# Optimization experiments

Measured on AMD Instinct MI355X. Metric: run time of the kernel, lower is better.

Reference implementation:

```python
import jax, jax.numpy as jnp
import numpy as np
from functools import reduce

N_QUBITS = 5
DIM = 2 ** N_QUBITS  # 32


def _cnot_np(c, t):
    # CNOT on N_QUBITS qubits, wire 0 = most significant bit (deepquantum convention)
    M = np.zeros((DIM, DIM), np.complex64)
    for i in range(DIM):
        if (i >> (N_QUBITS - 1 - c)) & 1:
            j = i ^ (1 << (N_QUBITS - 1 - t))
        else:
            j = i
        M[j, i] = 1.0
    return M

_CNOT = {(c, t): jnp.asarray(_cnot_np(c, t))
         for c in range(N_QUBITS) for t in range(N_QUBITS) if c != t}
_EYE2 = jnp.eye(2, dtype=jnp.complex64)


def _ry(theta):
    c = jnp.cos(theta / 2).astype(jnp.complex64)
    s = jnp.sin(theta / 2).astype(jnp.complex64)
    return jnp.stack([jnp.stack([c, -s]), jnp.stack([s, c])])


def _rx(theta):
    c = jnp.cos(theta / 2).astype(jnp.complex64)
    s = jnp.sin(theta / 2).astype(jnp.complex64)
    js = jnp.complex64(1j) * s
    return jnp.stack([jnp.stack([c, -js]), jnp.stack([-js, c])])


def _layer(gate_fn, thetas, wires):
    # kron of single-qubit gates on `wires`, identity elsewhere
    mats, idx = [], 0
    for w in range(N_QUBITS):
        if w in wires:
            mats.append(gate_fn(thetas[idx])); idx += 1
        else:
            mats.append(_EYE2)
    return reduce(jnp.kron, mats)


def _build_circuit(params, wires):
    # params: (n_blocks, 2, len(wires)); block = rylayer, rxlayer, then CNOTs
    # with control = block index and targets = all other wires in increasing order
    U = jnp.eye(DIM, dtype=jnp.complex64)
    n_blocks = params.shape[0]
    for b in range(n_blocks):
        U = _layer(_ry, params[b, 0], wires) @ U
        U = _layer(_rx, params[b, 1], wires) @ U
        for t in wires:
            if t != b:
                U = _CNOT[(b, t)] @ U
    return U


def setup_inputs() -> dict:
    key = jax.random.key(0)
    k1, k2, k3 = jax.random.split(key, 3)
    B = 65536
    oracles = jax.random.normal(k1, (B, DIM, DIM), dtype=jnp.float32)
    params1 = jax.random.normal(k2, (5, 2, 5), dtype=jnp.float32)  # cir1: 5 blocks, ry+rx, 5 wires
    params2 = jax.random.normal(k3, (4, 2, 4), dtype=jnp.float32)  # cir2: 4 blocks, ry+rx, wires [0,1,2,3]
    return {"oracles": oracles, "params1": params1, "params2": params2}


def reference(oracles, params1, params2):
    U1 = _build_circuit(params1, [0, 1, 2, 3, 4])
    U2 = _build_circuit(params2, [0, 1, 2, 3])
    psi1 = U1[:, 0]  # cir1 applied to |00000>
    mid = jnp.einsum('bij,j->bi', oracles.astype(jnp.complex64), psi1)  # oracle application (batched)
    fin = jnp.einsum('ij,bj->bi', U2, mid)                              # cir2
    x = jnp.abs(fin[:, 0]) ** 2 + jnp.abs(fin[:, 1]) ** 2
    return jnp.stack([x, 1.0 - x], axis=-1)  # (B, 2)
```

## Files before the change

### kernel.cpp

```cpp
#include <hip/hip_runtime.h>
#include <math.h>


__device__ __forceinline__ void apply_ry(float c, float s, int mask, int lane,
                                         float& re, float& im) {
    float pre = __shfl_xor(re, mask, 64);
    float pim = __shfl_xor(im, mask, 64);
    float sg = (lane & mask) ? s : -s;
    re = c * re + sg * pre;
    im = c * im + sg * pim;
}

__device__ __forceinline__ void apply_rx(float c, float s, int mask,
                                         float& re, float& im) {
    float pre = __shfl_xor(re, mask, 64);
    float pim = __shfl_xor(im, mask, 64);
    float nre = c * re + s * pim;
    float nim = c * im - s * pre;
    re = nre; im = nim;
}

__device__ __forceinline__ void apply_cnot(int cmask, int tmask, int lane,
                                           float& re, float& im) {
    float pre = __shfl_xor(re, tmask, 64);
    float pim = __shfl_xor(im, tmask, 64);
    if (lane & cmask) { re = pre; im = pim; }
}

__device__ __forceinline__ void u2row(const float* __restrict__ p2, int r,
                                      int lane, float& re, float& im) {
    re = ((lane & 31) == r) ? 1.f : 0.f;
    im = 0.f;
    for (int b = 3; b >= 0; --b) {
        for (int t = 3; t >= 0; --t)
            if (t != b) apply_cnot(1 << (4 - b), 1 << (4 - t), lane, re, im);
        for (int w = 0; w < 4; ++w) {
            float s, c; __sincosf(p2[b * 8 + 4 + w] * 0.5f, &s, &c);
            apply_rx(c, s, 1 << (4 - w), re, im);
        }
        for (int w = 0; w < 4; ++w) {
            float s, c; __sincosf(p2[b * 8 + w] * 0.5f, &s, &c);
            apply_ry(c, -s, 1 << (4 - w), lane, re, im);
        }
    }
}

__global__ __launch_bounds__(256, 4) void fused_kernel(const float* __restrict__ O,
                                                       const float* __restrict__ p1,
                                                       const float* __restrict__ p2,
                                                       float* __restrict__ out,
                                                       int nbatch) {
    const int lane = threadIdx.x & 63;
    const int wid = blockIdx.x * (blockDim.x >> 6) + (threadIdx.x >> 6);
    const int nw = gridDim.x * (blockDim.x >> 6);

    int b = wid;
    float4 cur[4], nxt[4];
    const bool has0 = b < nbatch;
    const bool has1 = b + nw < nbatch;
    if (has0) {
        const float4* row = (const float4*)(O + (size_t)b * 1024);
#pragma unroll
        for (int c = 0; c < 4; ++c) cur[c] = row[c * 64 + lane];
    }
    if (has1) {
        const float4* row = (const float4*)(O + (size_t)(b + nw) * 1024);
#pragma unroll
        for (int c = 0; c < 4; ++c) nxt[c] = row[c * 64 + lane];
    }

    float p_re = ((lane & 31) == 0) ? 1.f : 0.f, p_im = 0.f;
    for (int bb = 0; bb < 5; ++bb) {
        for (int w = 0; w < 5; ++w) {
            float s, c; __sincosf(p1[bb * 10 + w] * 0.5f, &s, &c);
            apply_ry(c, s, 1 << (4 - w), lane, p_re, p_im);
        }
        for (int w = 0; w < 5; ++w) {
            float s, c; __sincosf(p1[bb * 10 + 5 + w] * 0.5f, &s, &c);
            apply_rx(c, s, 1 << (4 - w), p_re, p_im);
        }
        for (int t = 0; t < 5; ++t)
            if (t != bb) apply_cnot(1 << (4 - bb), 1 << (4 - t), lane, p_re, p_im);
    }
    float r0re, r0im, r1re, r1im;
    u2row(p2, 0, lane, r0re, r0im);
    u2row(p2, 1, lane, r1re, r1im);

    float4 cf[4][4];
#pragma unroll
    for (int k = 0; k < 4; ++k) {
        const int e4 = 4 * lane + k;
        const int j = e4 & 31;
        const int tq = e4 >> 5;
        float pr = __shfl(p_re, j, 64);
        float pi = __shfl(p_im, j, 64);
#pragma unroll
        for (int c = 0; c < 4; ++c) {
            const int i = 8 * c + tq;
            float ar = __shfl(r0re, i, 64);
            float ai = __shfl(r0im, i, 64);
            float br = __shfl(r1re, i, 64);
            float bi = __shfl(r1im, i, 64);
            cf[c][k] = make_float4(ar * pr - ai * pi, ar * pi + ai * pr,
                                   br * pr - bi * pi, br * pi + bi * pr);
        }
    }

    if (!has0) return;

    while (true) {
        float a0 = 0.f, a1 = 0.f, a2 = 0.f, a3 = 0.f;
#pragma unroll
        for (int c = 0; c < 4; ++c) {
            float4 o = cur[c];
            a0 += o.x * cf[c][0].x + o.y * cf[c][1].x + o.z * cf[c][2].x + o.w * cf[c][3].x;
            a1 += o.x * cf[c][0].y + o.y * cf[c][1].y + o.z * cf[c][2].y + o.w * cf[c][3].y;
            a2 += o.x * cf[c][0].z + o.y * cf[c][1].z + o.z * cf[c][2].z + o.w * cf[c][3].z;
            a3 += o.x * cf[c][0].w + o.y * cf[c][1].w + o.z * cf[c][2].w + o.w * cf[c][3].w;
        }

        float v01 = (lane & 1) ? a1 : a0;
        float o01 = (lane & 1) ? a0 : a1;
        v01 += __shfl_xor(o01, 1, 64);
        float v23 = (lane & 1) ? a3 : a2;
        float o23 = (lane & 1) ? a2 : a3;
        v23 += __shfl_xor(o23, 1, 64);
        float v = (lane & 2) ? v23 : v01;
        float ov = (lane & 2) ? v01 : v23;
        v += __shfl_xor(ov, 2, 64);
#pragma unroll
        for (int m = 4; m < 64; m <<= 1) v += __shfl_xor(v, m, 64);
        float x = v * v;
        x += __shfl_xor(x, 1, 64);
        x += __shfl_xor(x, 2, 64);
        if (lane == 0) ((float2*)out)[b] = make_float2(x, 1.0f - x);

        b += nw;
        if (b >= nbatch) break;
#pragma unroll
        for (int c = 0; c < 4; ++c) cur[c] = nxt[c];
        if (b + nw < nbatch) {
            const float4* row = (const float4*)(O + (size_t)(b + nw) * 1024);
#pragma unroll
            for (int c = 0; c < 4; ++c) nxt[c] = row[c * 64 + lane];
        }
    }
}

extern "C" void kernel_launch(void* const* d_in, const int* in_sizes, int n_in,
                              void* d_out, int out_size, void* d_ws, size_t ws_size,
                              hipStream_t stream) {
    const float* oracles = (const float*)d_in[0];
    const float* p1 = (const float*)d_in[1];
    const float* p2 = (const float*)d_in[2];
    float* out = (float*)d_out;
    int nbatch = in_sizes[0] / 1024;

    fused_kernel<<<1024, 256, 0, stream>>>(oracles, p1, p2, out, nbatch);
}
```

Baseline: 51.16 us.

## Deepen row prefetch to three buffers, use contiguous per-wave ranges and fp16 dot2

Each wave now takes a contiguous range of batch rows instead of a grid-strided set. It keeps three rows of loads in flight with nontemporal loads and stores, where before it had one row prefetched. The oracle values and coefficients are packed to fp16 and reduced with fdot2, which cuts register use and ALU work in the inner loop. The two U2 rows are also computed in a single pass by splitting them across the two half-waves. Converting to fp16 with round-toward-zero loses precision compared with the fp32 reference.

```diff
diff --git a/kernel.cpp b/kernel.cpp
--- a/kernel.cpp
+++ b/kernel.cpp
@@ -1,6 +1,20 @@
 #include <hip/hip_runtime.h>
 #include <math.h>
 
+
+typedef __fp16 h2 __attribute__((ext_vector_type(2)));
+typedef float f4 __attribute__((ext_vector_type(4)));
+typedef float f2 __attribute__((ext_vector_type(2)));
+
+#if __has_builtin(__builtin_amdgcn_fdot2)
+#define FDOT2(a, b, c) __builtin_amdgcn_fdot2((a), (b), (c), false)
+#else
+#define FDOT2(a, b, c) ((c) + (float)(a)[0] * (float)(b)[0] + (float)(a)[1] * (float)(b)[1])
+#endif
+
+__device__ __forceinline__ h2 pkrtz(float x, float y) {
+    return __builtin_amdgcn_cvt_pkrtz(x, y);
+}
 
 __device__ __forceinline__ void apply_ry(float c, float s, int mask, int lane,
                                          float& re, float& im) {
@@ -27,23 +41,51 @@
     if (lane & cmask) { re = pre; im = pim; }
 }
 
-__device__ __forceinline__ void u2row(const float* __restrict__ p2, int r,
-                                      int lane, float& re, float& im) {
-    re = ((lane & 31) == r) ? 1.f : 0.f;
-    im = 0.f;
-    for (int b = 3; b >= 0; --b) {
-        for (int t = 3; t >= 0; --t)
-            if (t != b) apply_cnot(1 << (4 - b), 1 << (4 - t), lane, re, im);
-        for (int w = 0; w < 4; ++w) {
-            float s, c; __sincosf(p2[b * 8 + 4 + w] * 0.5f, &s, &c);
-            apply_rx(c, s, 1 << (4 - w), re, im);
-        }
-        for (int w = 0; w < 4; ++w) {
-            float s, c; __sincosf(p2[b * 8 + w] * 0.5f, &s, &c);
-            apply_ry(c, -s, 1 << (4 - w), lane, re, im);
-        }
+struct CF { h2 v[4][4][2]; };
+
+__device__ __forceinline__ void process(const f4& w0, const f4& w1,
+                                        const f4& w2, const f4& w3,
+                                        const CF& cf, int lane, size_t bb,
+                                        float* __restrict__ out) {
+    h2 o[4][2];
+    o[0][0] = pkrtz(w0.x, w0.y); o[0][1] = pkrtz(w0.z, w0.w);
+    o[1][0] = pkrtz(w1.x, w1.y); o[1][1] = pkrtz(w1.z, w1.w);
+    o[2][0] = pkrtz(w2.x, w2.y); o[2][1] = pkrtz(w2.z, w2.w);
+    o[3][0] = pkrtz(w3.x, w3.y); o[3][1] = pkrtz(w3.z, w3.w);
+    float a0 = 0.f, a1 = 0.f, a2 = 0.f, a3 = 0.f;
+#pragma unroll
+    for (int c = 0; c < 4; ++c) {
+        a0 = FDOT2(o[c][0], cf.v[c][0][0], a0); a0 = FDOT2(o[c][1], cf.v[c][0][1], a0);
+        a1 = FDOT2(o[c][0], cf.v[c][1][0], a1); a1 = FDOT2(o[c][1], cf.v[c][1][1], a1);
+        a2 = FDOT2(o[c][0], cf.v[c][2][0], a2); a2 = FDOT2(o[c][1], cf.v[c][2][1], a2);
+        a3 = FDOT2(o[c][0], cf.v[c][3][0], a3); a3 = FDOT2(o[c][1], cf.v[c][3][1], a3);
+    }
+    float v01 = (lane & 1) ? a1 : a0;
+    float q01 = (lane & 1) ? a0 : a1;
+    v01 += __shfl_xor(q01, 1, 64);
+    float v23 = (lane & 1) ? a3 : a2;
+    float q23 = (lane & 1) ? a2 : a3;
+    v23 += __shfl_xor(q23, 1, 64);
+    float v = (lane & 2) ? v23 : v01;
+    float qv = (lane & 2) ? v01 : v23;
+    v += __shfl_xor(qv, 2, 64);
+#pragma unroll
+    for (int m = 4; m < 64; m <<= 1) v += __shfl_xor(v, m, 64);
+    float x = v * v;
+    x += __shfl_xor(x, 1, 64);
+    x += __shfl_xor(x, 2, 64);
+    if (lane == 0) {
+        f2 res; res.x = x; res.y = 1.0f - x;
+        __builtin_nontemporal_store(res, (f2*)out + bb);
     }
 }
+
+#define LOADROW(P0, P1, P2, P3, bb) do { if ((size_t)(bb) < end) {           \
+    const f4* r_ = (const f4*)(O + (size_t)(bb) * 1024) + lane;              \
+    P0 = __builtin_nontemporal_load(r_);                                     \
+    P1 = __builtin_nontemporal_load(r_ + 64);                                \
+    P2 = __builtin_nontemporal_load(r_ + 128);                               \
+    P3 = __builtin_nontemporal_load(r_ + 192); } } while (0)
 
 __global__ __launch_bounds__(256, 4) void fused_kernel(const float* __restrict__ O,
                                                        const float* __restrict__ p1,
@@ -54,20 +96,13 @@
     const int wid = blockIdx.x * (blockDim.x >> 6) + (threadIdx.x >> 6);
     const int nw = gridDim.x * (blockDim.x >> 6);
 
-    int b = wid;
-    float4 cur[4], nxt[4];
-    const bool has0 = b < nbatch;
-    const bool has1 = b + nw < nbatch;
-    if (has0) {
-        const float4* row = (const float4*)(O + (size_t)b * 1024);
-#pragma unroll
-        for (int c = 0; c < 4; ++c) cur[c] = row[c * 64 + lane];
-    }
-    if (has1) {
-        const float4* row = (const float4*)(O + (size_t)(b + nw) * 1024);
-#pragma unroll
-        for (int c = 0; c < 4; ++c) nxt[c] = row[c * 64 + lane];
-    }
+    const size_t start = (size_t)wid * (size_t)nbatch / nw;
+    const size_t end = (size_t)(wid + 1) * (size_t)nbatch / nw;
+
+    f4 A0, A1, A2, A3, B0, B1, B2, B3, C0, C1, C2, C3;
+    LOADROW(A0, A1, A2, A3, start);
+    LOADROW(B0, B1, B2, B3, start + 1);
+    LOADROW(C0, C1, C2, C3, start + 2);
 
     float p_re = ((lane & 31) == 0) ? 1.f : 0.f, p_im = 0.f;
     for (int bb = 0; bb < 5; ++bb) {
@@ -82,67 +117,58 @@
         for (int t = 0; t < 5; ++t)
             if (t != bb) apply_cnot(1 << (4 - bb), 1 << (4 - t), lane, p_re, p_im);
     }
-    float r0re, r0im, r1re, r1im;
-    u2row(p2, 0, lane, r0re, r0im);
-    u2row(p2, 1, lane, r1re, r1im);
 
-    float4 cf[4][4];
-#pragma unroll
-    for (int k = 0; k < 4; ++k) {
-        const int e4 = 4 * lane + k;
-        const int j = e4 & 31;
-        const int tq = e4 >> 5;
-        float pr = __shfl(p_re, j, 64);
-        float pi = __shfl(p_im, j, 64);
-#pragma unroll
-        for (int c = 0; c < 4; ++c) {
-            const int i = 8 * c + tq;
-            float ar = __shfl(r0re, i, 64);
-            float ai = __shfl(r0im, i, 64);
-            float br = __shfl(r1re, i, 64);
-            float bi = __shfl(r1im, i, 64);
-            cf[c][k] = make_float4(ar * pr - ai * pi, ar * pi + ai * pr,
-                                   br * pr - bi * pi, br * pi + bi * pr);
+    float r_re = ((lane & 31) == (lane >> 5)) ? 1.f : 0.f, r_im = 0.f;
+    for (int bb = 3; bb >= 0; --bb) {
+        for (int t = 3; t >= 0; --t)
+            if (t != bb) apply_cnot(1 << (4 - bb), 1 << (4 - t), lane, r_re, r_im);
+        for (int w = 0; w < 4; ++w) {
+            float s, c; __sincosf(p2[bb * 8 + 4 + w] * 0.5f, &s, &c);
+            apply_rx(c, s, 1 << (4 - w), r_re, r_im);
+        }
+        for (int w = 0; w < 4; ++w) {
+            float s, c; __sincosf(p2[bb * 8 + w] * 0.5f, &s, &c);
+            apply_ry(c, -s, 1 << (4 - w), lane, r_re, r_im);
         }
     }
 
-    if (!has0) return;
+    const int tq = (lane >> 3) & 7;
+    const int j0 = (4 * lane) & 31;
+    float pr[4], pi[4];
+#pragma unroll
+    for (int k = 0; k < 4; ++k) {
+        pr[k] = __shfl(p_re, j0 + k, 64);
+        pi[k] = __shfl(p_im, j0 + k, 64);
+    }
+    CF cf;
+#pragma unroll
+    for (int c = 0; c < 4; ++c) {
+        const int i = 8 * c + tq;
+        float ar = __shfl(r_re, i, 64),      ai = __shfl(r_im, i, 64);
+        float br = __shfl(r_re, 32 + i, 64), bi = __shfl(r_im, 32 + i, 64);
+#pragma unroll
+        for (int h = 0; h < 2; ++h) {
+            const int k = 2 * h;
+            cf.v[c][0][h] = pkrtz(ar * pr[k] - ai * pi[k], ar * pr[k + 1] - ai * pi[k + 1]);
+            cf.v[c][1][h] = pkrtz(ar * pi[k] + ai * pr[k], ar * pi[k + 1] + ai * pr[k + 1]);
+            cf.v[c][2][h] = pkrtz(br * pr[k] - bi * pi[k], br * pr[k + 1] - bi * pi[k + 1]);
+            cf.v[c][3][h] = pkrtz(br * pi[k] + bi * pr[k], br * pi[k + 1] + bi * pr[k + 1]);
+        }
+    }
 
-    while (true) {
-        float a0 = 0.f, a1 = 0.f, a2 = 0.f, a3 = 0.f;
-#pragma unroll
-        for (int c = 0; c < 4; ++c) {
-            float4 o = cur[c];
-            a0 += o.x * cf[c][0].x + o.y * cf[c][1].x + o.z * cf[c][2].x + o.w * cf[c][3].x;
-            a1 += o.x * cf[c][0].y + o.y * cf[c][1].y + o.z * cf[c][2].y + o.w * cf[c][3].y;
-            a2 += o.x * cf[c][0].z + o.y * cf[c][1].z + o.z * cf[c][2].z + o.w * cf[c][3].z;
-            a3 += o.x * cf[c][0].w + o.y * cf[c][1].w + o.z * cf[c][2].w + o.w * cf[c][3].w;
-        }
-
-        float v01 = (lane & 1) ? a1 : a0;
-        float o01 = (lane & 1) ? a0 : a1;
-        v01 += __shfl_xor(o01, 1, 64);
-        float v23 = (lane & 1) ? a3 : a2;
-        float o23 = (lane & 1) ? a2 : a3;
-        v23 += __shfl_xor(o23, 1, 64);
-        float v = (lane & 2) ? v23 : v01;
-        float ov = (lane & 2) ? v01 : v23;
-        v += __shfl_xor(ov, 2, 64);
-#pragma unroll
-        for (int m = 4; m < 64; m <<= 1) v += __shfl_xor(v, m, 64);
-        float x = v * v;
-        x += __shfl_xor(x, 1, 64);
-        x += __shfl_xor(x, 2, 64);
-        if (lane == 0) ((float2*)out)[b] = make_float2(x, 1.0f - x);
-
-        b += nw;
-        if (b >= nbatch) break;
-#pragma unroll
-        for (int c = 0; c < 4; ++c) cur[c] = nxt[c];
-        if (b + nw < nbatch) {
-            const float4* row = (const float4*)(O + (size_t)(b + nw) * 1024);
-#pragma unroll
-            for (int c = 0; c < 4; ++c) nxt[c] = row[c * 64 + lane];
+    size_t b = start;
+    if (b < end) {
+        for (;;) {
+            process(A0, A1, A2, A3, cf, lane, b, out);
+            LOADROW(A0, A1, A2, A3, b + 3);
+            if (b + 1 >= end) break;
+            process(B0, B1, B2, B3, cf, lane, b + 1, out);
+            LOADROW(B0, B1, B2, B3, b + 4);
+            if (b + 2 >= end) break;
+            process(C0, C1, C2, C3, cf, lane, b + 2, out);
+            LOADROW(C0, C1, C2, C3, b + 5);
+            b += 3;
+            if (b >= end) break;
         }
     }
 }
```

Result: slower. 55.01 us (+7.5%).
